# Kernel tuning notes

Hardware: AMD Instinct MI355X
Metric: run time of the kernel (lower is better)

## Reference

```python
import jax, jax.numpy as jnp
import numpy as np

N_NODES = 50000
N_EDGES = 800000
DIM_IN = 128
DIM_OUT = 64
HEADS = 4
NEG_SLOPE = 0.2


def setup_inputs() -> dict:
    key = jax.random.key(0)
    k_x, k_e, k_w, k_a = jax.random.split(key, 4)
    x = jax.random.normal(k_x, (N_NODES, DIM_IN), dtype=jnp.float32)
    edge_index = jax.random.randint(k_e, (2, N_EDGES), 0, N_NODES, dtype=jnp.int32)
    # Stacked per-head params: W (Linear(dim_in, dim_out, bias=False)) and
    # a (Linear(2*dim_out, 1, bias=False)) for each of HEADS heads.
    W = jax.random.normal(k_w, (HEADS, DIM_IN, DIM_OUT), dtype=jnp.float32) * (1.0 / np.sqrt(DIM_IN))
    a = jax.random.normal(k_a, (HEADS, 2 * DIM_OUT), dtype=jnp.float32) * (1.0 / np.sqrt(2 * DIM_OUT))
    return {"x": x, "edge_index": edge_index, "W": W, "a": a}


def _gat_forward(x, W, a, edge_index):
    src = edge_index[0]  # segment for softmax / scatter target
    dst = edge_index[1]  # node whose features are gathered (x_j)
    # h: [N, H, D]
    h = jnp.einsum('nd,hdo->nho', x, W)
    a_i = a[:, :DIM_OUT]   # [H, D] applied to x_i
    a_j = a[:, DIM_OUT:]   # [H, D] applied to x_j
    # per-node attention logit halves: [N, H]
    s_i = jnp.einsum('nhd,hd->nh', h, a_i)
    s_j = jnp.einsum('nhd,hd->nh', h, a_j)
    e = jax.nn.leaky_relu(s_i[src] + s_j[dst], NEG_SLOPE)  # [E, H]
    # segment softmax over edges grouped by src node
    m = jax.ops.segment_max(e, src, num_segments=N_NODES)  # [N, H]
    ex = jnp.exp(e - m[src])
    denom = jax.ops.segment_sum(ex, src, num_segments=N_NODES)  # [N, H]
    att = ex / denom[src]  # [E, H]
    # weighted scatter-sum of gathered features: [N, H, D]
    msgs = att[:, :, None] * h[dst]
    h_prime = jax.ops.segment_sum(msgs, src, num_segments=N_NODES)
    # concat=False -> mean over heads
    return jnp.mean(h_prime, axis=1)  # [N, D]


def reference(x, edge_index, W, a):
    return _gat_forward(x, W, a, edge_index)
```

## Files before the change

### kernel.cpp

```cpp
#include <hip/hip_runtime.h>
#include <hip/hip_bf16.h>

#define N_NODES 50000
#define N_EDGES 800000
#define DIM_IN  128
#define DIM_OUT 64
#define HEADS   4
#define NEG_SLOPE 0.2f
#define NPB 32
#define GEMM_BLOCKS ((N_NODES + NPB - 1) / NPB)
#define N_PAD (GEMM_BLOCKS * NPB)
#define PAD 64
#define CHUNKS 128
#define EPC (N_EDGES / CHUNKS)
#define RANGES 128
#define RSPAN 391
#define OPITCH 132
#define XROW 136
#define LTROW 260
#define SMEM_BYTES (2 * NPB * XROW * 2)

typedef __attribute__((ext_vector_type(8))) short short8;
typedef __attribute__((ext_vector_type(4))) short short4v;
typedef __attribute__((ext_vector_type(4))) float f32x4;

__device__ __forceinline__ unsigned int f2bf(float f) {
    unsigned int u = __float_as_uint(f);
    return (u + 0x7FFFu + ((u >> 16) & 1u)) >> 16;
}
__device__ __forceinline__ float bf2f(unsigned int b) {
    return __uint_as_float(b << 16);
}

__device__ __forceinline__ void packW_role(
    int i, const float* __restrict__ W,
    unsigned short* __restrict__ Wph, unsigned short* __restrict__ Wpl)
{
    const int lane = i & 63, nt = (i >> 6) & 3, kc = (i >> 8) & 3, h = (i >> 10) & 3;
    const int col = lane & 15, quad = lane >> 4;
    unsigned short hv[8], lv[8];
#pragma unroll
    for (int j = 0; j < 8; ++j) {
        const int k = kc * 32 + quad * 8 + j;
        const int n = nt * 16 + col;
        const float f = W[h * (DIM_IN * DIM_OUT) + k * DIM_OUT + n];
        const unsigned int hb = f2bf(f);
        hv[j] = (unsigned short)hb;
        lv[j] = (unsigned short)f2bf(f - bf2f(hb));
    }
    *(short8*)(Wph + (size_t)i * 8) = *(short8*)hv;
    *(short8*)(Wpl + (size_t)i * 8) = *(short8*)lv;
}

__global__ __launch_bounds__(512) void sort_kernel(
    const float* __restrict__ W, unsigned short* __restrict__ Wph,
    unsigned short* __restrict__ Wpl, const int* __restrict__ ei,
    unsigned int* __restrict__ offT, unsigned int* __restrict__ ebuf)
{
    const int b = blockIdx.x;
    const int t = threadIdx.x;
    if (b < 8) { packW_role(b * 512 + t, W, Wph, Wpl); return; }

    __shared__ unsigned int hist[RANGES];
    __shared__ unsigned int scn[RANGES + 1];
    __shared__ unsigned int cur[RANGES];
    const int c = b - 8;
    if (t < RANGES) hist[t] = 0u;
    __syncthreads();
    const int* srcp = ei + c * EPC;
    const int* dstp = ei + N_EDGES + c * EPC;
    for (int e = t; e < EPC; e += 512) atomicAdd(&hist[srcp[e] / RSPAN], 1u);
    __syncthreads();
    if (t < RANGES) scn[t + 1] = hist[t];
    if (t == 0) scn[0] = 0u;
    __syncthreads();
    for (int off = 1; off < RANGES; off <<= 1) {
        unsigned int v = 0u;
        if (t < RANGES && (t + 1) > off) v = scn[t + 1 - off];
        __syncthreads();
        if (t < RANGES) scn[t + 1] += v;
        __syncthreads();
    }
    if (t < RANGES) {
        cur[t] = scn[t];
        offT[c * OPITCH + t] = (unsigned int)(c * EPC) + scn[t];
    }
    if (t == 0) offT[c * OPITCH + RANGES] = (unsigned int)((c + 1) * EPC);
    __syncthreads();
    unsigned int* eb = ebuf + (size_t)c * EPC;
    for (int e = t; e < EPC; e += 512) {
        const int s = srcp[e];
        const int d = dstp[e];
        const int r = s / RSPAN;
        const unsigned int pos = atomicAdd(&cur[r], 1u);
        eb[pos] = ((unsigned int)(s - r * RSPAN) << 16) | (unsigned int)d;
    }
}

__device__ __forceinline__ void gemm_role(
    int nb, int t, const float* __restrict__ x,
    const unsigned short* __restrict__ Wph, const unsigned short* __restrict__ Wpl,
    const float* __restrict__ a, unsigned short* __restrict__ h2,
    float* __restrict__ s_i, float* __restrict__ s_j, void* smemv)
{
    short* xh = (short*)smemv;
    short* xl = xh + NPB * XROW;

    {
        const float4* xg = (const float4*)x;
        const int base = nb * (DIM_IN / 4);
        const int limit = N_NODES * (DIM_IN / 4);
#pragma unroll
        for (int r = 0; r < 4; ++r) {
            const int idx = t + 256 * r;
            const int gi = base + idx;
            float4 v = {0.f, 0.f, 0.f, 0.f};
            if (gi < limit) v = xg[gi];
            const int node = idx >> 5;
            const int dg = (idx & 31) * 4;
            unsigned short hs[4], ls[4];
            const float fv[4] = {v.x, v.y, v.z, v.w};
#pragma unroll
            for (int c = 0; c < 4; ++c) {
                const unsigned int hb = f2bf(fv[c]);
                hs[c] = (unsigned short)hb;
                ls[c] = (unsigned short)f2bf(fv[c] - bf2f(hb));
            }
            *(short4v*)(xh + node * XROW + dg) = *(short4v*)hs;
            *(short4v*)(xl + node * XROW + dg) = *(short4v*)ls;
        }
    }
    __syncthreads();

    const int w = t >> 6;
    const int lane = t & 63;
    const int col = lane & 15, quad = lane >> 4;

    f32x4 acc[2][4];
#pragma unroll
    for (int mt = 0; mt < 2; ++mt)
#pragma unroll
        for (int nt = 0; nt < 4; ++nt) acc[mt][nt] = (f32x4){0.f, 0.f, 0.f, 0.f};

    const short8* Bh = (const short8*)Wph;
    const short8* Bl = (const short8*)Wpl;
#pragma unroll
    for (int kc = 0; kc < 4; ++kc) {
        const short8 ah0 = *(const short8*)(xh + (0 * 16 + col) * XROW + kc * 32 + quad * 8);
        const short8 al0 = *(const short8*)(xl + (0 * 16 + col) * XROW + kc * 32 + quad * 8);
        const short8 ah1 = *(const short8*)(xh + (1 * 16 + col) * XROW + kc * 32 + quad * 8);
        const short8 al1 = *(const short8*)(xl + (1 * 16 + col) * XROW + kc * 32 + quad * 8);
#pragma unroll
        for (int nt = 0; nt < 4; ++nt) {
            const int fi = ((w * 4 + kc) * 4 + nt) * 64 + lane;
            const short8 bh = Bh[fi];
            const short8 bl = Bl[fi];
            acc[0][nt] = __builtin_amdgcn_mfma_f32_16x16x32_bf16(ah0, bh, acc[0][nt], 0, 0, 0);
            acc[0][nt] = __builtin_amdgcn_mfma_f32_16x16x32_bf16(al0, bh, acc[0][nt], 0, 0, 0);
            acc[0][nt] = __builtin_amdgcn_mfma_f32_16x16x32_bf16(ah0, bl, acc[0][nt], 0, 0, 0);
            acc[1][nt] = __builtin_amdgcn_mfma_f32_16x16x32_bf16(ah1, bh, acc[1][nt], 0, 0, 0);
            acc[1][nt] = __builtin_amdgcn_mfma_f32_16x16x32_bf16(al1, bh, acc[1][nt], 0, 0, 0);
            acc[1][nt] = __builtin_amdgcn_mfma_f32_16x16x32_bf16(ah1, bl, acc[1][nt], 0, 0, 0);
        }
    }

    float aiv[4], ajv[4];
#pragma unroll
    for (int nt = 0; nt < 4; ++nt) {
        aiv[nt] = a[w * (2 * DIM_OUT) + nt * 16 + col];
        ajv[nt] = a[w * (2 * DIM_OUT) + DIM_OUT + nt * 16 + col];
    }
#pragma unroll
    for (int mt = 0; mt < 2; ++mt) {
#pragma unroll
        for (int r = 0; r < 4; ++r) {
            float pi = 0.f, pj = 0.f;
#pragma unroll
            for (int nt = 0; nt < 4; ++nt) {
                pi = fmaf(acc[mt][nt][r], aiv[nt], pi);
                pj = fmaf(acc[mt][nt][r], ajv[nt], pj);
            }
#pragma unroll
            for (int off = 8; off > 0; off >>= 1) {
                pi += __shfl_down(pi, off, 16);
                pj += __shfl_down(pj, off, 16);
            }
            if (col == 0) {
                const int n = nb + mt * 16 + quad * 4 + r;
                s_i[n * HEADS + w] = pi;
                s_j[n * HEADS + w] = pj;
            }
        }
    }
    __syncthreads();

    short* lt = (short*)smemv;
#pragma unroll
    for (int mt = 0; mt < 2; ++mt)
#pragma unroll
        for (int nt = 0; nt < 4; ++nt)
#pragma unroll
            for (int r = 0; r < 4; ++r)
                lt[(mt * 16 + quad * 4 + r) * LTROW + (nt * 16 + col) * 4 + w] =
                    (short)f2bf(acc[mt][nt][r]);
    __syncthreads();

    uint2* hg = (uint2*)(h2 + (size_t)nb * (DIM_OUT * HEADS));
#pragma unroll
    for (int r = 0; r < 8; ++r) {
        const int idx = t + 256 * r;
        const int node = idx >> 6;
        const int wo = idx & 63;
        hg[idx] = *(const uint2*)(lt + node * LTROW + wo * 4);
    }
}

__global__ __launch_bounds__(256) void csr_gemm_kernel(
    const float* __restrict__ x, const unsigned short* __restrict__ Wph,
    const unsigned short* __restrict__ Wpl, const float* __restrict__ a,
    unsigned short* __restrict__ h2, float* __restrict__ s_i, float* __restrict__ s_j,
    const unsigned int* __restrict__ offT, const unsigned int* __restrict__ ebuf,
    unsigned short* __restrict__ sdst, int* __restrict__ cursor)
{
    __shared__ __align__(16) unsigned char smem[SMEM_BYTES];
    const int b = blockIdx.x;
    const int t = threadIdx.x;

    if (b < RANGES) {
        unsigned int* cur  = (unsigned int*)smem;
        unsigned int* offA = cur + RSPAN;
        unsigned int* offB = offA + CHUNKS;
        const int r = b;
        for (int i = t; i < RSPAN; i += 256) cur[i] = 0u;
        if (t < CHUNKS) {
            offA[t] = offT[t * OPITCH + r];
            offB[t] = offT[t * OPITCH + r + 1];
        }
        __syncthreads();
        const int w = t >> 6, lane = t & 63;
        for (int c = w; c < CHUNKS; c += 4) {
            const unsigned int j0 = offA[c], j1 = offB[c];
            for (unsigned int e = j0 + lane; e < j1; e += 64) {
                const unsigned int v = ebuf[e];
                const unsigned int sl = v >> 16;
                const unsigned int d = v & 0xFFFFu;
                const unsigned int slot = atomicAdd(&cur[sl], 1u);
                if (slot < PAD) sdst[(size_t)(r * RSPAN + sl) * PAD + slot] = (unsigned short)d;
            }
        }
        __syncthreads();
        for (int i = t; i < RSPAN; i += 256) {
            const int n = r * RSPAN + i;
            if (n < N_NODES) cursor[n] = (int)cur[i];
        }
        return;
    }

    gemm_role((b - RANGES) * NPB, t, x, Wph, Wpl, a, h2, s_i, s_j, smem);
}

__global__ __launch_bounds__(256) void fused_kernel(
    const int* __restrict__ cursor, const unsigned short* __restrict__ sdst,
    const float* __restrict__ s_i, const float* __restrict__ s_j,
    const unsigned short* __restrict__ h2, float* __restrict__ out)
{
    __shared__ float4 att_s[4][64];
    __shared__ int    dst_s[4][64];
    const int w = (threadIdx.x >> 6) & 3;
    const int lane = threadIdx.x & 63;
    const int n = blockIdx.x * 4 + w;
    if (n >= N_NODES) return;
    const int d = min(cursor[n], PAD);
    const int start = n * PAD;

    float acc = 0.f;
    if (d > 0) {
        const float4 si = *(const float4*)(s_i + n * HEADS);
        float4 m4 = {-INFINITY, -INFINITY, -INFINITY, -INFINITY};
        float4 cz = {-INFINITY, -INFINITY, -INFINITY, -INFINITY};
        int cdst = 0;
        if (lane < d) {
            cdst = (int)sdst[start + lane];
            const float4 sj = *(const float4*)(s_j + cdst * HEADS);
            float z0 = si.x + sj.x, z1 = si.y + sj.y, z2 = si.z + sj.z, z3 = si.w + sj.w;
            cz.x = z0 >= 0.f ? z0 : NEG_SLOPE * z0;
            cz.y = z1 >= 0.f ? z1 : NEG_SLOPE * z1;
            cz.z = z2 >= 0.f ? z2 : NEG_SLOPE * z2;
            cz.w = z3 >= 0.f ? z3 : NEG_SLOPE * z3;
            m4 = cz;
        }
#pragma unroll
        for (int off = 32; off > 0; off >>= 1) {
            m4.x = fmaxf(m4.x, __shfl_xor(m4.x, off, 64));
            m4.y = fmaxf(m4.y, __shfl_xor(m4.y, off, 64));
            m4.z = fmaxf(m4.z, __shfl_xor(m4.z, off, 64));
            m4.w = fmaxf(m4.w, __shfl_xor(m4.w, off, 64));
        }
        float4 ex = {0.f, 0.f, 0.f, 0.f};
        if (lane < d) {
            ex.x = __expf(cz.x - m4.x);
            ex.y = __expf(cz.y - m4.y);
            ex.z = __expf(cz.z - m4.z);
            ex.w = __expf(cz.w - m4.w);
        }
        float4 sm = ex;
#pragma unroll
        for (int off = 32; off > 0; off >>= 1) {
            sm.x += __shfl_xor(sm.x, off, 64);
            sm.y += __shfl_xor(sm.y, off, 64);
            sm.z += __shfl_xor(sm.z, off, 64);
            sm.w += __shfl_xor(sm.w, off, 64);
        }
        if (lane < d) {
            att_s[w][lane] = make_float4(ex.x / sm.x, ex.y / sm.y, ex.z / sm.z, ex.w / sm.w);
            dst_s[w][lane] = cdst;
        }

        const unsigned short* hbase = h2 + lane * HEADS;
        int e = 0;
        for (; e + 8 <= d; e += 8) {
            uint2 hv[8];
            float4 at[8];
#pragma unroll
            for (int q = 0; q < 8; ++q) {
                const int dd = dst_s[w][e + q];
                at[q] = att_s[w][e + q];
                hv[q] = *(const uint2*)(hbase + (size_t)dd * (DIM_OUT * HEADS));
            }
#pragma unroll
            for (int q = 0; q < 8; ++q) {
                acc += at[q].x * bf2f(hv[q].x & 0xFFFFu) + at[q].y * bf2f(hv[q].x >> 16)
                     + at[q].z * bf2f(hv[q].y & 0xFFFFu) + at[q].w * bf2f(hv[q].y >> 16);
            }
        }
        for (; e + 4 <= d; e += 4) {
            uint2 hv[4];
            float4 at[4];
#pragma unroll
            for (int q = 0; q < 4; ++q) {
                const int dd = dst_s[w][e + q];
                at[q] = att_s[w][e + q];
                hv[q] = *(const uint2*)(hbase + (size_t)dd * (DIM_OUT * HEADS));
            }
#pragma unroll
            for (int q = 0; q < 4; ++q) {
                acc += at[q].x * bf2f(hv[q].x & 0xFFFFu) + at[q].y * bf2f(hv[q].x >> 16)
                     + at[q].z * bf2f(hv[q].y & 0xFFFFu) + at[q].w * bf2f(hv[q].y >> 16);
            }
        }
        for (; e < d; ++e) {
            const int dd = dst_s[w][e];
            const float4 a4 = att_s[w][e];
            const uint2 hv = *(const uint2*)(hbase + (size_t)dd * (DIM_OUT * HEADS));
            acc += a4.x * bf2f(hv.x & 0xFFFFu) + a4.y * bf2f(hv.x >> 16)
                 + a4.z * bf2f(hv.y & 0xFFFFu) + a4.w * bf2f(hv.y >> 16);
        }
    }
    out[n * DIM_OUT + lane] = 0.25f * acc;
}

extern "C" void kernel_launch(void* const* d_in, const int* in_sizes, int n_in,
                              void* d_out, int out_size, void* d_ws, size_t ws_size,
                              hipStream_t stream) {
    const float* x  = (const float*)d_in[0];
    const int*   ei = (const int*)d_in[1];
    const float* W  = (const float*)d_in[2];
    const float* a  = (const float*)d_in[3];
    float* out = (float*)d_out;

    char* ws = (char*)d_ws;
    size_t off = 0;
    auto alloc = [&](size_t bytes) { void* p = ws + off; off = (off + bytes + 511) & ~size_t(511); return p; };
    unsigned short* h2  = (unsigned short*)alloc(sizeof(unsigned short) * N_PAD * DIM_OUT * HEADS);
    float* s_i    = (float*)alloc(sizeof(float) * N_PAD * HEADS);
    float* s_j    = (float*)alloc(sizeof(float) * N_PAD * HEADS);
    int*   cursor = (int*)alloc(sizeof(int) * N_NODES);
    unsigned short* sdst = (unsigned short*)alloc(sizeof(unsigned short) * N_NODES * PAD);
    unsigned int* offT   = (unsigned int*)alloc(sizeof(unsigned int) * CHUNKS * OPITCH);
    unsigned int* ebuf   = (unsigned int*)alloc(sizeof(unsigned int) * N_EDGES);
    unsigned short* Wph  = (unsigned short*)alloc(sizeof(unsigned short) * HEADS * DIM_IN * DIM_OUT);
    unsigned short* Wpl  = (unsigned short*)alloc(sizeof(unsigned short) * HEADS * DIM_IN * DIM_OUT);

    sort_kernel<<<8 + CHUNKS, 512, 0, stream>>>(W, Wph, Wpl, ei, offT, ebuf);

    csr_gemm_kernel<<<RANGES + GEMM_BLOCKS, 256, 0, stream>>>(
        x, Wph, Wpl, a, h2, s_i, s_j, offT, ebuf, sdst, cursor);

    const int fb = (N_NODES + 3) / 4;
    fused_kernel<<<fb, 256, 0, stream>>>(cursor, sdst, s_i, s_j, h2, out);
}
```

Before: 169.8 us.

## Store degree inline in padded CSR row and prefetch first gather before softmax

Result: no change. 167.7 us (-1.3%).

```diff
diff --git a/kernel.cpp b/kernel.cpp
--- a/kernel.cpp
+++ b/kernel.cpp
@@ -11,6 +11,7 @@
 #define GEMM_BLOCKS ((N_NODES + NPB - 1) / NPB)
 #define N_PAD (GEMM_BLOCKS * NPB)
 #define PAD 64
+#define MAXD 63
 #define CHUNKS 128
 #define EPC (N_EDGES / CHUNKS)
 #define RANGES 128
@@ -220,7 +221,7 @@
     const unsigned short* __restrict__ Wpl, const float* __restrict__ a,
     unsigned short* __restrict__ h2, float* __restrict__ s_i, float* __restrict__ s_j,
     const unsigned int* __restrict__ offT, const unsigned int* __restrict__ ebuf,
-    unsigned short* __restrict__ sdst, int* __restrict__ cursor)
+    unsigned short* __restrict__ sdst)
 {
     __shared__ __align__(16) unsigned char smem[SMEM_BYTES];
     const int b = blockIdx.x;
@@ -245,13 +246,13 @@
                 const unsigned int sl = v >> 16;
                 const unsigned int d = v & 0xFFFFu;
                 const unsigned int slot = atomicAdd(&cur[sl], 1u);
-                if (slot < PAD) sdst[(size_t)(r * RSPAN + sl) * PAD + slot] = (unsigned short)d;
+                if (slot < MAXD) sdst[(size_t)(r * RSPAN + sl) * PAD + 1 + slot] = (unsigned short)d;
             }
         }
         __syncthreads();
         for (int i = t; i < RSPAN; i += 256) {
             const int n = r * RSPAN + i;
-            if (n < N_NODES) cursor[n] = (int)cur[i];
+            if (n < N_NODES) sdst[(size_t)n * PAD] = (unsigned short)min(cur[i], (unsigned int)MAXD);
         }
         return;
     }
@@ -260,7 +261,7 @@
 }
 
 __global__ __launch_bounds__(256) void fused_kernel(
-    const int* __restrict__ cursor, const unsigned short* __restrict__ sdst,
+    const unsigned short* __restrict__ sdst,
     const float* __restrict__ s_i, const float* __restrict__ s_j,
     const unsigned short* __restrict__ h2, float* __restrict__ out)
 {
@@ -270,93 +271,79 @@
     const int lane = threadIdx.x & 63;
     const int n = blockIdx.x * 4 + w;
     if (n >= N_NODES) return;
-    const int d = min(cursor[n], PAD);
-    const int start = n * PAD;
-
-    float acc = 0.f;
-    if (d > 0) {
-        const float4 si = *(const float4*)(s_i + n * HEADS);
-        float4 m4 = {-INFINITY, -INFINITY, -INFINITY, -INFINITY};
-        float4 cz = {-INFINITY, -INFINITY, -INFINITY, -INFINITY};
-        int cdst = 0;
-        if (lane < d) {
-            cdst = (int)sdst[start + lane];
-            const float4 sj = *(const float4*)(s_j + cdst * HEADS);
-            float z0 = si.x + sj.x, z1 = si.y + sj.y, z2 = si.z + sj.z, z3 = si.w + sj.w;
-            cz.x = z0 >= 0.f ? z0 : NEG_SLOPE * z0;
-            cz.y = z1 >= 0.f ? z1 : NEG_SLOPE * z1;
-            cz.z = z2 >= 0.f ? z2 : NEG_SLOPE * z2;
-            cz.w = z3 >= 0.f ? z3 : NEG_SLOPE * z3;
-            m4 = cz;
-        }
-#pragma unroll
-        for (int off = 32; off > 0; off >>= 1) {
-            m4.x = fmaxf(m4.x, __shfl_xor(m4.x, off, 64));
-            m4.y = fmaxf(m4.y, __shfl_xor(m4.y, off, 64));
-            m4.z = fmaxf(m4.z, __shfl_xor(m4.z, off, 64));
-            m4.w = fmaxf(m4.w, __shfl_xor(m4.w, off, 64));
-        }
-        float4 ex = {0.f, 0.f, 0.f, 0.f};
-        if (lane < d) {
-            ex.x = __expf(cz.x - m4.x);
-            ex.y = __expf(cz.y - m4.y);
-            ex.z = __expf(cz.z - m4.z);
-            ex.w = __expf(cz.w - m4.w);
-        }
-        float4 sm = ex;
-#pragma unroll
-        for (int off = 32; off > 0; off >>= 1) {
-            sm.x += __shfl_xor(sm.x, off, 64);
-            sm.y += __shfl_xor(sm.y, off, 64);
-            sm.z += __shfl_xor(sm.z, off, 64);
-            sm.w += __shfl_xor(sm.w, off, 64);
-        }
-        if (lane < d) {
-            att_s[w][lane] = make_float4(ex.x / sm.x, ex.y / sm.y, ex.z / sm.z, ex.w / sm.w);
-            dst_s[w][lane] = cdst;
-        }
-
-        const unsigned short* hbase = h2 + lane * HEADS;
-        int e = 0;
-        for (; e + 8 <= d; e += 8) {
-            uint2 hv[8];
-            float4 at[8];
-#pragma unroll
-            for (int q = 0; q < 8; ++q) {
-                const int dd = dst_s[w][e + q];
-                at[q] = att_s[w][e + q];
-                hv[q] = *(const uint2*)(hbase + (size_t)dd * (DIM_OUT * HEADS));
-            }
-#pragma unroll
-            for (int q = 0; q < 8; ++q) {
-                acc += at[q].x * bf2f(hv[q].x & 0xFFFFu) + at[q].y * bf2f(hv[q].x >> 16)
-                     + at[q].z * bf2f(hv[q].y & 0xFFFFu) + at[q].w * bf2f(hv[q].y >> 16);
-            }
-        }
-        for (; e + 4 <= d; e += 4) {
-            uint2 hv[4];
-            float4 at[4];
-#pragma unroll
-            for (int q = 0; q < 4; ++q) {
-                const int dd = dst_s[w][e + q];
-                at[q] = att_s[w][e + q];
-                hv[q] = *(const uint2*)(hbase + (size_t)dd * (DIM_OUT * HEADS));
-            }
-#pragma unroll
-            for (int q = 0; q < 4; ++q) {
-                acc += at[q].x * bf2f(hv[q].x & 0xFFFFu) + at[q].y * bf2f(hv[q].x >> 16)
-                     + at[q].z * bf2f(hv[q].y & 0xFFFFu) + at[q].w * bf2f(hv[q].y >> 16);
-            }
-        }
-        for (; e < d; ++e) {
-            const int dd = dst_s[w][e];
-            const float4 a4 = att_s[w][e];
-            const uint2 hv = *(const uint2*)(hbase + (size_t)dd * (DIM_OUT * HEADS));
-            acc += a4.x * bf2f(hv.x & 0xFFFFu) + a4.y * bf2f(hv.x >> 16)
-                 + a4.z * bf2f(hv.y & 0xFFFFu) + a4.w * bf2f(hv.y >> 16);
-        }
-    }
-    out[n * DIM_OUT + lane] = 0.25f * acc;
+
+    const int myv = (int)sdst[(size_t)n * PAD + lane];
+    const int d = __shfl(myv, 0, 64);
+
+    if (d == 0) { out[n * DIM_OUT + lane] = 0.f; return; }
+
+    att_s[w][lane] = make_float4(0.f, 0.f, 0.f, 0.f);
+    dst_s[w][lane] = 0;
+    const bool has_edge = (lane >= 1) && (lane <= d);
+    if (has_edge) dst_s[w][lane - 1] = myv;
+
+    const unsigned short* hbase = h2 + lane * HEADS;
+    uint2 hv[8];
+#pragma unroll
+    for (int q = 0; q < 8; ++q)
+        hv[q] = *(const uint2*)(hbase + (size_t)dst_s[w][q] * (DIM_OUT * HEADS));
+
+    const float4 si = *(const float4*)(s_i + n * HEADS);
+    float4 m4 = {-INFINITY, -INFINITY, -INFINITY, -INFINITY};
+    float4 cz = {-INFINITY, -INFINITY, -INFINITY, -INFINITY};
+    if (has_edge) {
+        const float4 sj = *(const float4*)(s_j + myv * HEADS);
+        float z0 = si.x + sj.x, z1 = si.y + sj.y, z2 = si.z + sj.z, z3 = si.w + sj.w;
+        cz.x = z0 >= 0.f ? z0 : NEG_SLOPE * z0;
+        cz.y = z1 >= 0.f ? z1 : NEG_SLOPE * z1;
+        cz.z = z2 >= 0.f ? z2 : NEG_SLOPE * z2;
+        cz.w = z3 >= 0.f ? z3 : NEG_SLOPE * z3;
+        m4 = cz;
+    }
+#pragma unroll
+    for (int off = 32; off > 0; off >>= 1) {
+        m4.x = fmaxf(m4.x, __shfl_xor(m4.x, off, 64));
+        m4.y = fmaxf(m4.y, __shfl_xor(m4.y, off, 64));
+        m4.z = fmaxf(m4.z, __shfl_xor(m4.z, off, 64));
+        m4.w = fmaxf(m4.w, __shfl_xor(m4.w, off, 64));
+    }
+    float4 ex = {0.f, 0.f, 0.f, 0.f};
+    if (has_edge) {
+        ex.x = __expf(cz.x - m4.x);
+        ex.y = __expf(cz.y - m4.y);
+        ex.z = __expf(cz.z - m4.z);
+        ex.w = __expf(cz.w - m4.w);
+    }
+    float4 sm = ex;
+#pragma unroll
+    for (int off = 32; off > 0; off >>= 1) {
+        sm.x += __shfl_xor(sm.x, off, 64);
+        sm.y += __shfl_xor(sm.y, off, 64);
+        sm.z += __shfl_xor(sm.z, off, 64);
+        sm.w += __shfl_xor(sm.w, off, 64);
+    }
+    if (has_edge) att_s[w][lane - 1] = ex;
+
+    float a0 = 0.f, a1 = 0.f, a2 = 0.f, a3 = 0.f;
+    const int nb8 = (d + 7) >> 3;
+    int bb = 0;
+    while (true) {
+#pragma unroll
+        for (int q = 0; q < 8; ++q) {
+            const float4 at = att_s[w][bb * 8 + q];
+            const uint2 v = hv[q];
+            a0 = fmaf(at.x, __uint_as_float(v.x << 16), a0);
+            a1 = fmaf(at.y, __uint_as_float(v.x & 0xFFFF0000u), a1);
+            a2 = fmaf(at.z, __uint_as_float(v.y << 16), a2);
+            a3 = fmaf(at.w, __uint_as_float(v.y & 0xFFFF0000u), a3);
+        }
+        if (++bb >= nb8) break;
+#pragma unroll
+        for (int q = 0; q < 8; ++q)
+            hv[q] = *(const uint2*)(hbase + (size_t)dst_s[w][bb * 8 + q] * (DIM_OUT * HEADS));
+    }
+
+    out[n * DIM_OUT + lane] = 0.25f * (a0 / sm.x + a1 / sm.y + a2 / sm.z + a3 / sm.w);
 }
 
 extern "C" void kernel_launch(void* const* d_in, const int* in_sizes, int n_in,
@@ -374,7 +361,6 @@
     unsigned short* h2  = (unsigned short*)alloc(sizeof(unsigned short) * N_PAD * DIM_OUT * HEADS);
     float* s_i    = (float*)alloc(sizeof(float) * N_PAD * HEADS);
     float* s_j    = (float*)alloc(sizeof(float) * N_PAD * HEADS);
-    int*   cursor = (int*)alloc(sizeof(int) * N_NODES);
     unsigned short* sdst = (unsigned short*)alloc(sizeof(unsigned short) * N_NODES * PAD);
     unsigned int* offT   = (unsigned int*)alloc(sizeof(unsigned int) * CHUNKS * OPITCH);
     unsigned int* ebuf   = (unsigned int*)alloc(sizeof(unsigned int) * N_EDGES);
@@ -384,8 +370,8 @@
     sort_kernel<<<8 + CHUNKS, 512, 0, stream>>>(W, Wph, Wpl, ei, offT, ebuf);
 
     csr_gemm_kernel<<<RANGES + GEMM_BLOCKS, 256, 0, stream>>>(
-        x, Wph, Wpl, a, h2, s_i, s_j, offT, ebuf, sdst, cursor);
+        x, Wph, Wpl, a, h2, s_i, s_j, offT, ebuf, sdst);
 
     const int fb = (N_NODES + 3) / 4;
-    fused_kernel<<<fb, 256, 0, stream>>>(cursor, sdst, s_i, s_j, h2, out);
-}
+    fused_kernel<<<fb, 256, 0, stream>>>(sdst, s_i, s_j, h2, out);
+}
```
